# Kernel optimization log

Measured on AMD Instinct MI355X. Metric: run time of the kernel, lower is better.

The kernel has to match this reference:

```python
import jax, jax.numpy as jnp
import numpy as np

B, S, DM, NH, DK, DFF = 4, 2048, 512, 8, 64, 2048
EPS = 1e-5


def setup_inputs() -> dict:
    key = jax.random.key(0)
    ks = jax.random.split(key, 16)
    sd = 1.0 / np.sqrt(DM)
    inp = {
        'x': jax.random.normal(ks[0], (B, S, DM), dtype=jnp.float32),
        'wq': jax.random.normal(ks[1], (DM, DM), dtype=jnp.float32) * sd,
        'bq': jnp.zeros((DM,), dtype=jnp.float32),
        'wk': jax.random.normal(ks[2], (DM, DM), dtype=jnp.float32) * sd,
        'bk': jnp.zeros((DM,), dtype=jnp.float32),
        'wv': jax.random.normal(ks[3], (DM, DM), dtype=jnp.float32) * sd,
        'bv': jnp.zeros((DM,), dtype=jnp.float32),
        'wo': jax.random.normal(ks[4], (DM, DM), dtype=jnp.float32) * sd,
        'bo': jnp.zeros((DM,), dtype=jnp.float32),
        'ln_g': jnp.ones((DM,), dtype=jnp.float32),
        'ln_b': jnp.zeros((DM,), dtype=jnp.float32),
        'w1': jax.random.normal(ks[5], (DFF, DM), dtype=jnp.float32) * sd,
        'b1': jnp.zeros((DFF,), dtype=jnp.float32),
        'w2': jax.random.normal(ks[6], (DM, DFF), dtype=jnp.float32) * (1.0 / np.sqrt(DFF)),
        'b2': jnp.zeros((DM,), dtype=jnp.float32),
    }
    return inp


def _layernorm(x, g, b):
    mu = jnp.mean(x, axis=-1, keepdims=True)
    var = jnp.mean(jnp.square(x - mu), axis=-1, keepdims=True)
    return (x - mu) * jax.lax.rsqrt(var + EPS) * g + b


def reference(x, wq, bq, wk, bk, wv, bv, wo, bo, ln_g, ln_b, w1, b1, w2, b2):
    # projections (torch Linear: y = x @ W.T + b)
    q = x @ wq.T + bq
    k = x @ wk.T + bk
    v = x @ wv.T + bv
    # chunk along feature dim into NH heads of size DK
    q = q.reshape(B, S, NH, DK)
    k = k.reshape(B, S, NH, DK)
    v = v.reshape(B, S, NH, DK)
    scores = jnp.einsum('bihd,bjhd->bhij', q, k) / np.sqrt(DK)  # [B,NH,S,S]
    probs = jax.nn.softmax(scores, axis=-1)
    o = jnp.einsum('bhij,bjhd->bihd', probs, v).reshape(B, S, DM)
    o = o @ wo.T + bo
    # residual + shared layernorm (dropout p=0 -> identity)
    h = _layernorm(o + x, ln_g, ln_b)
    ff = jax.nn.relu(h @ w1.T + b1) @ w2.T + b2
    return _layernorm(ff + h, ln_g, ln_b)
```

## Files before the change

kernel.cpp:

```cpp
#include <hip/hip_runtime.h>

typedef __attribute__((ext_vector_type(8))) short short8;
typedef __attribute__((ext_vector_type(8))) unsigned short ushort8;
typedef __attribute__((ext_vector_type(4))) unsigned short ushort4v;
typedef __attribute__((ext_vector_type(4))) float f32x4;
typedef __attribute__((ext_vector_type(16))) float f32x16;

#define DEV static __device__ __forceinline__

DEV unsigned short f2bf(float f) {
  unsigned u = __builtin_bit_cast(unsigned, f);
  u += 0x7fffu + ((u >> 16) & 1u);
  return (unsigned short)(u >> 16);
}

DEV float bf2f(unsigned short u) {
  return __builtin_bit_cast(float, (unsigned)u << 16);
}

DEV void gload_lds16(const void* g, void* l) {
  __builtin_amdgcn_global_load_lds((__attribute__((address_space(1))) void*)g,
                                   (__attribute__((address_space(3))) void*)l,
                                   16, 0, 0);
}

DEV unsigned cvtpk(float lo, float hi) {
  unsigned u;
  asm("v_cvt_pk_bf16_f32 %0, %1, %2" : "=v"(u) : "v"(lo), "v"(hi));
  return u;
}

DEV void pl32(unsigned& a, unsigned& b) {
  asm("v_permlane32_swap_b32 %0, %1" : "+v"(a), "+v"(b));
}

DEV short8 pack4(unsigned a, unsigned b, unsigned c, unsigned d) {
  int4 t = make_int4((int)a, (int)b, (int)c, (int)d);
  return __builtin_bit_cast(short8, t);
}

__global__ __launch_bounds__(256) void cvt_all_k(
    const float4* __restrict__ wq, const float4* __restrict__ wk,
    const float4* __restrict__ wv, const float4* __restrict__ wo,
    const float4* __restrict__ w1, const float4* __restrict__ w2,
    const float4* __restrict__ x, ushort4v* __restrict__ wqkv,
    ushort4v* __restrict__ wob, ushort4v* __restrict__ w1b,
    ushort4v* __restrict__ w2b, ushort4v* __restrict__ xb) {
  const int i = threadIdx.x;
  const int b = blockIdx.x;
  const float4* s;
  ushort4v* d;
  size_t u;
  if (b < 256)       { s = wq; d = wqkv;          u = (size_t)b * 256 + i; }
  else if (b < 512)  { s = wk; d = wqkv + 65536;  u = (size_t)(b - 256) * 256 + i; }
  else if (b < 768)  { s = wv; d = wqkv + 131072; u = (size_t)(b - 512) * 256 + i; }
  else if (b < 1024) { s = wo; d = wob;           u = (size_t)(b - 768) * 256 + i; }
  else if (b < 2048) { s = w1; d = w1b;           u = (size_t)(b - 1024) * 256 + i; }
  else if (b < 3072) { s = w2; d = w2b;           u = (size_t)(b - 2048) * 256 + i; }
  else               { s = x;  d = xb;            u = (size_t)(b - 3072) * 256 + i; }
  float4 v = s[u];
  ushort4v o = { f2bf(v.x), f2bf(v.y), f2bf(v.z), f2bf(v.w) };
  d[u] = o;
}

__global__ void pack_bias_k(const float* __restrict__ bq, const float* __restrict__ bk,
                            const float* __restrict__ bv, float* __restrict__ o) {
  int i = threadIdx.x;
  o[i] = bq[i];
  o[512 + i] = bk[i];
  o[1024 + i] = bv[i];
}

template <int EPI>
__global__ __launch_bounds__(256) void gemm_bt(
    const unsigned short* __restrict__ A, const unsigned short* __restrict__ Bw,
    const float* __restrict__ bias, int M, int N, int K,
    unsigned short* __restrict__ outb, float* __restrict__ outf,
    const unsigned short* __restrict__ residb) {
  __shared__ __align__(16) unsigned short As[128 * 64];
  __shared__ __align__(16) unsigned short Bs[128 * 64];
  const int tid = threadIdx.x;
  const int lane = tid & 63;
  const int wv = tid >> 6;
  const int wr = wv >> 1, wc = wv & 1;
  const int lrow = lane & 15, lgrp = lane >> 4;
  const int bm = blockIdx.x * 128;
  const int bn = blockIdx.y * 128;

  f32x4 acc[4][4];
#pragma unroll
  for (int m = 0; m < 4; m++)
#pragma unroll
    for (int n = 0; n < 4; n++) acc[m][n] = (f32x4){0.f, 0.f, 0.f, 0.f};

  for (int k0 = 0; k0 < K; k0 += 64) {
    __syncthreads();
#pragma unroll
    for (int i = 0; i < 4; i++) {
      const int sb = wv * 64 + i * 256;
      const int slot = sb + lane;
      const int row = slot >> 3;
      const int cc = (slot & 7) ^ (row & 7);
      gload_lds16(A + (size_t)(bm + row) * K + k0 + cc * 8, &As[sb * 8]);
      gload_lds16(Bw + (size_t)(bn + row) * K + k0 + cc * 8, &Bs[sb * 8]);
    }
    __syncthreads();

#pragma unroll
    for (int kk = 0; kk < 2; kk++) {
      short8 af[4], bfr[4];
#pragma unroll
      for (int m = 0; m < 4; m++) {
        const int row = wr * 64 + m * 16 + lrow;
        af[m] = *(const short8*)&As[row * 64 + (((lgrp + 4 * kk) ^ (row & 7)) * 8)];
      }
#pragma unroll
      for (int n = 0; n < 4; n++) {
        const int row = wc * 64 + n * 16 + lrow;
        bfr[n] = *(const short8*)&Bs[row * 64 + (((lgrp + 4 * kk) ^ (row & 7)) * 8)];
      }
#pragma unroll
      for (int m = 0; m < 4; m++)
#pragma unroll
        for (int n = 0; n < 4; n++)
          acc[m][n] = __builtin_amdgcn_mfma_f32_16x16x32_bf16(af[m], bfr[n], acc[m][n], 0, 0, 0);
    }
  }

  if constexpr (EPI == 0) {
    const int proj = bn >> 9;
    if (proj == 2) {
      __shared__ __align__(16) unsigned short VT[128 * 136];
#pragma unroll
      for (int n = 0; n < 4; n++) {
        const int cl = wc * 64 + n * 16 + lrow;
        const float bval = bias[bn + cl];
#pragma unroll
        for (int m = 0; m < 4; m++)
#pragma unroll
          for (int r = 0; r < 4; r++)
            VT[cl * 136 + wr * 64 + m * 16 + lgrp * 4 + r] = f2bf(acc[m][n][r] + bval);
      }
      __syncthreads();
      const int j = (bn - 1024) >> 7;
      const int b = bm >> 11;
      const int sbase = bm & 2047;
      unsigned short* vout = outb + (size_t)2 * 4194304;
#pragma unroll
      for (int q = 0; q < 8; q++) {
        const int chunk = q * 256 + tid;
        const int cl = chunk >> 4, s8 = chunk & 15;
        const int head = 2 * j + (cl >> 6), d = cl & 63;
        ushort8 val = *(const ushort8*)&VT[cl * 136 + s8 * 8];
        *(ushort8*)(vout + ((size_t)(b * 8 + head) * 64 + d) * 2048 + sbase + s8 * 8) = val;
      }
    } else {
      const float qs = (proj == 0) ? 0.18033688011f : 1.0f;
#pragma unroll
      for (int m = 0; m < 4; m++) {
#pragma unroll
        for (int n = 0; n < 4; n++) {
          const int gcol = bn + wc * 64 + n * 16 + lrow;
          const float bval = bias[gcol];
          const int feat = gcol & 511;
          const int head = feat >> 6, d = feat & 63;
#pragma unroll
          for (int r = 0; r < 4; r++) {
            const int grow = bm + wr * 64 + m * 16 + lgrp * 4 + r;
            const int b = grow >> 11, s = grow & 2047;
            const int bh = b * 8 + head;
            outb[(size_t)proj * 4194304 + ((size_t)bh * 2048 + s) * 64 + d] =
                f2bf((acc[m][n][r] + bval) * qs);
          }
        }
      }
    }
  } else {
#pragma unroll
    for (int m = 0; m < 4; m++) {
#pragma unroll
      for (int n = 0; n < 4; n++) {
        const int gcol = bn + wc * 64 + n * 16 + lrow;
        const float bval = bias[gcol];
#pragma unroll
        for (int r = 0; r < 4; r++) {
          const int grow = bm + wr * 64 + m * 16 + lgrp * 4 + r;
          float v = acc[m][n][r] + bval;
          const size_t o = (size_t)grow * N + gcol;
          if constexpr (EPI == 1) {
            outb[o] = f2bf(v + bf2f(residb[o]));
          } else if constexpr (EPI == 2) {
            outb[o] = f2bf(v > 0.f ? v : 0.f);
          } else {
            outf[o] = v + bf2f(residb[o]);
          }
        }
      }
    }
  }
}

template <int EPI>
__global__ __launch_bounds__(256) void gemm_n64(
    const unsigned short* __restrict__ A, const unsigned short* __restrict__ Bw,
    const float* __restrict__ bias, int M, int N, int K,
    unsigned short* __restrict__ outb, float* __restrict__ outf,
    const unsigned short* __restrict__ residb) {
  __shared__ __align__(16) unsigned short As[128 * 64];
  __shared__ __align__(16) unsigned short Bs[64 * 64];
  const int tid = threadIdx.x;
  const int lane = tid & 63;
  const int wv = tid >> 6;
  const int lrow = lane & 15, lgrp = lane >> 4;
  const int bm = blockIdx.x * 128;
  const int bn = blockIdx.y * 64;

  f32x4 acc[2][4];
#pragma unroll
  for (int m = 0; m < 2; m++)
#pragma unroll
    for (int n = 0; n < 4; n++) acc[m][n] = (f32x4){0.f, 0.f, 0.f, 0.f};

  for (int k0 = 0; k0 < K; k0 += 64) {
    __syncthreads();
#pragma unroll
    for (int i = 0; i < 4; i++) {
      const int sb = wv * 64 + i * 256;
      const int slot = sb + lane;
      const int row = slot >> 3;
      const int cc = (slot & 7) ^ (row & 7);
      gload_lds16(A + (size_t)(bm + row) * K + k0 + cc * 8, &As[sb * 8]);
    }
#pragma unroll
    for (int i = 0; i < 2; i++) {
      const int sb = wv * 64 + i * 256;
      const int slot = sb + lane;
      const int row = slot >> 3;
      const int cc = (slot & 7) ^ (row & 7);
      gload_lds16(Bw + (size_t)(bn + row) * K + k0 + cc * 8, &Bs[sb * 8]);
    }
    __syncthreads();

#pragma unroll
    for (int kk = 0; kk < 2; kk++) {
      short8 af[2], bfr[4];
#pragma unroll
      for (int m = 0; m < 2; m++) {
        const int row = wv * 32 + m * 16 + lrow;
        af[m] = *(const short8*)&As[row * 64 + (((lgrp + 4 * kk) ^ (row & 7)) * 8)];
      }
#pragma unroll
      for (int n = 0; n < 4; n++) {
        const int row = n * 16 + lrow;
        bfr[n] = *(const short8*)&Bs[row * 64 + (((lgrp + 4 * kk) ^ (row & 7)) * 8)];
      }
#pragma unroll
      for (int m = 0; m < 2; m++)
#pragma unroll
        for (int n = 0; n < 4; n++)
          acc[m][n] = __builtin_amdgcn_mfma_f32_16x16x32_bf16(af[m], bfr[n], acc[m][n], 0, 0, 0);
    }
  }

#pragma unroll
  for (int m = 0; m < 2; m++) {
#pragma unroll
    for (int n = 0; n < 4; n++) {
      const int gcol = bn + n * 16 + lrow;
      const float bval = bias[gcol];
#pragma unroll
      for (int r = 0; r < 4; r++) {
        const int grow = bm + wv * 32 + m * 16 + lgrp * 4 + r;
        float v = acc[m][n][r] + bval;
        const size_t o = (size_t)grow * N + gcol;
        if constexpr (EPI == 1) {
          outb[o] = f2bf(v + bf2f(residb[o]));
        } else {
          outf[o] = v + bf2f(residb[o]);
        }
      }
    }
  }
}

__global__ __launch_bounds__(256) void attn_k(
    const unsigned short* __restrict__ Qg, const unsigned short* __restrict__ Kg,
    const unsigned short* __restrict__ Vg, unsigned short* __restrict__ Og) {
  __shared__ __align__(16) unsigned short Kl[2][64 * 64];
  __shared__ __align__(16) unsigned short Vl[2][64 * 64];
  const int tid = threadIdx.x, lane = tid & 63, wq = tid >> 6;
  const int ql = lane & 31;
  const int hi = lane >> 5;
  const int bid = blockIdx.x;
  const int lin = (bid & 7) * 64 + (bid >> 3);
  const int bh = lin >> 4;
  const int q0 = (lin & 15) * 128;
  const int qw = q0 + wq * 32;
  const size_t hbase = (size_t)bh * (2048 * 64);

  const int sb0 = wq * 64, sb1 = wq * 64 + 256;
  const int r0s = (sb0 + lane) >> 3, c0s = ((sb0 + lane) & 7) ^ (r0s & 7);
  const int r1s = (sb1 + lane) >> 3, c1s = ((sb1 + lane) & 7) ^ (r1s & 7);

  short8 qreg[4];
  {
    const unsigned short* qp = Qg + hbase + (size_t)(qw + ql) * 64 + hi * 8;
#pragma unroll
    for (int i = 0; i < 4; i++) qreg[i] = *(const short8*)(qp + 16 * i);
  }

  f32x16 oac0 = {0.f, 0.f, 0.f, 0.f, 0.f, 0.f, 0.f, 0.f,
                 0.f, 0.f, 0.f, 0.f, 0.f, 0.f, 0.f, 0.f};
  f32x16 oac1 = oac0;
  float lr = 0.f;

  gload_lds16(Kg + hbase + (size_t)r0s * 64 + c0s * 8, &Kl[0][sb0 * 8]);
  gload_lds16(Vg + hbase + (size_t)r0s * 2048 + c0s * 8, &Vl[0][sb0 * 8]);
  gload_lds16(Kg + hbase + (size_t)r1s * 64 + c1s * 8, &Kl[0][sb1 * 8]);
  gload_lds16(Vg + hbase + (size_t)r1s * 2048 + c1s * 8, &Vl[0][sb1 * 8]);
  __syncthreads();

  for (int it = 0; it < 32; ++it) {
    const int cur = it & 1;
    if (it < 31) {
      const int kt = (it + 1) * 64;
      const int nxt = cur ^ 1;
      gload_lds16(Kg + hbase + (size_t)(kt + r0s) * 64 + c0s * 8, &Kl[nxt][sb0 * 8]);
      gload_lds16(Vg + hbase + (size_t)r0s * 2048 + kt + c0s * 8, &Vl[nxt][sb0 * 8]);
      gload_lds16(Kg + hbase + (size_t)(kt + r1s) * 64 + c1s * 8, &Kl[nxt][sb1 * 8]);
      gload_lds16(Vg + hbase + (size_t)r1s * 2048 + kt + c1s * 8, &Vl[nxt][sb1 * 8]);
    }

    f32x16 sc0 = {0.f, 0.f, 0.f, 0.f, 0.f, 0.f, 0.f, 0.f,
                  0.f, 0.f, 0.f, 0.f, 0.f, 0.f, 0.f, 0.f};
    f32x16 sc1 = sc0;
    __builtin_amdgcn_s_setprio(1);
#pragma unroll
    for (int i = 0; i < 4; i++) {
      const int c8 = 2 * i + hi;
      const int r0 = ql;
      const int r1 = ql + 32;
      short8 ka = *(const short8*)&Kl[cur][(r0 * 8 + (c8 ^ (r0 & 7))) * 8];
      short8 kb = *(const short8*)&Kl[cur][(r1 * 8 + (c8 ^ (r1 & 7))) * 8];
      sc0 = __builtin_amdgcn_mfma_f32_32x32x16_bf16(ka, qreg[i], sc0, 0, 0, 0);
      sc1 = __builtin_amdgcn_mfma_f32_32x32x16_bf16(kb, qreg[i], sc1, 0, 0, 0);
    }
    __builtin_amdgcn_s_setprio(0);

    short8 pa[4];
#pragma unroll
    for (int t2 = 0; t2 < 2; t2++) {
      const f32x16& sc = t2 ? sc1 : sc0;
      float p[16];
#pragma unroll
      for (int r = 0; r < 16; r++) {
        p[r] = __builtin_amdgcn_exp2f(sc[r]);
        lr += p[r];
      }
      unsigned w0a = cvtpk(p[0], p[1]),   w0b = cvtpk(p[2], p[3]);
      unsigned w1a = cvtpk(p[4], p[5]),   w1b = cvtpk(p[6], p[7]);
      unsigned w2a = cvtpk(p[8], p[9]),   w2b = cvtpk(p[10], p[11]);
      unsigned w3a = cvtpk(p[12], p[13]), w3b = cvtpk(p[14], p[15]);
      pl32(w0a, w1a);
      pl32(w0b, w1b);
      pa[2 * t2] = pack4(w0a, w0b, w1a, w1b);
      pl32(w2a, w3a);
      pl32(w2b, w3b);
      pa[2 * t2 + 1] = pack4(w2a, w2b, w3a, w3b);
    }

    __builtin_amdgcn_s_setprio(1);
#pragma unroll
    for (int ks = 0; ks < 4; ks++) {
      const int c8 = 2 * ks + hi;
      const int r0 = ql;
      const int r1 = ql + 32;
      short8 vb0 = *(const short8*)&Vl[cur][(r0 * 8 + (c8 ^ (r0 & 7))) * 8];
      short8 vb1 = *(const short8*)&Vl[cur][(r1 * 8 + (c8 ^ (r1 & 7))) * 8];
      oac0 = __builtin_amdgcn_mfma_f32_32x32x16_bf16(pa[ks], vb0, oac0, 0, 0, 0);
      oac1 = __builtin_amdgcn_mfma_f32_32x32x16_bf16(pa[ks], vb1, oac1, 0, 0, 0);
    }
    __builtin_amdgcn_s_setprio(0);

    __syncthreads();
  }

  lr += __shfl_xor(lr, 32);
  const float inv = 1.0f / lr;

  const int b = bh >> 3, h = bh & 7;
#pragma unroll
  for (int r = 0; r < 16; r++) {
    const int qrow = (r & 3) + 8 * (r >> 2) + 4 * hi;
    const float invr = __shfl(inv, qrow);
    const size_t base = ((size_t)(b * 2048 + qw + qrow)) * 512 + h * 64 + ql;
    Og[base] = f2bf(oac0[r] * invr);
    Og[base + 32] = f2bf(oac1[r] * invr);
  }
}

__global__ __launch_bounds__(64) void ln_k(const float* __restrict__ in,
                                           const float* __restrict__ g,
                                           const float* __restrict__ bb,
                                           float* __restrict__ outf) {
  const int row = blockIdx.x, lane = threadIdx.x;
  const float4* p = (const float4*)(in + (size_t)row * 512);
  float4 a = p[lane], b4 = p[lane + 64];
  float s = a.x + a.y + a.z + a.w + b4.x + b4.y + b4.z + b4.w;
#pragma unroll
  for (int off = 32; off >= 1; off >>= 1) s += __shfl_xor(s, off);
  const float mu = s * (1.f / 512.f);
  float q = 0.f;
  {
    float d;
    d = a.x - mu; q += d * d; d = a.y - mu; q += d * d;
    d = a.z - mu; q += d * d; d = a.w - mu; q += d * d;
    d = b4.x - mu; q += d * d; d = b4.y - mu; q += d * d;
    d = b4.z - mu; q += d * d; d = b4.w - mu; q += d * d;
  }
#pragma unroll
  for (int off = 32; off >= 1; off >>= 1) q += __shfl_xor(q, off);
  const float rstd = rsqrtf(q * (1.f / 512.f) + 1e-5f);
  const float4* gp = (const float4*)g;
  const float4* bp = (const float4*)bb;
  float4 g0 = gp[lane], g1 = gp[lane + 64], c0 = bp[lane], c1 = bp[lane + 64];
  float4 o0, o1;
  o0.x = (a.x - mu) * rstd * g0.x + c0.x;
  o0.y = (a.y - mu) * rstd * g0.y + c0.y;
  o0.z = (a.z - mu) * rstd * g0.z + c0.z;
  o0.w = (a.w - mu) * rstd * g0.w + c0.w;
  o1.x = (b4.x - mu) * rstd * g1.x + c1.x;
  o1.y = (b4.y - mu) * rstd * g1.y + c1.y;
  o1.z = (b4.z - mu) * rstd * g1.z + c1.z;
  o1.w = (b4.w - mu) * rstd * g1.w + c1.w;
  float4* of = (float4*)(outf + (size_t)row * 512);
  of[lane] = o0;
  of[lane + 64] = o1;
}

__global__ __launch_bounds__(64) void ln_bf_k(const unsigned short* __restrict__ in,
                                              const float* __restrict__ g,
                                              const float* __restrict__ bb,
                                              unsigned short* __restrict__ out) {
  const int row = blockIdx.x, lane = threadIdx.x;
  ushort8 v = *(const ushort8*)(in + (size_t)row * 512 + lane * 8);
  float f[8];
#pragma unroll
  for (int j = 0; j < 8; j++) f[j] = bf2f(v[j]);
  float s = 0.f;
#pragma unroll
  for (int j = 0; j < 8; j++) s += f[j];
#pragma unroll
  for (int off = 32; off >= 1; off >>= 1) s += __shfl_xor(s, off);
  const float mu = s * (1.f / 512.f);
  float q = 0.f;
#pragma unroll
  for (int j = 0; j < 8; j++) { const float d = f[j] - mu; q += d * d; }
#pragma unroll
  for (int off = 32; off >= 1; off >>= 1) q += __shfl_xor(q, off);
  const float rstd = rsqrtf(q * (1.f / 512.f) + 1e-5f);
  const float4* gp = (const float4*)g;
  const float4* bp = (const float4*)bb;
  float4 g0 = gp[lane * 2], g1 = gp[lane * 2 + 1];
  float4 c0 = bp[lane * 2], c1 = bp[lane * 2 + 1];
  const float gg[8] = {g0.x, g0.y, g0.z, g0.w, g1.x, g1.y, g1.z, g1.w};
  const float cc[8] = {c0.x, c0.y, c0.z, c0.w, c1.x, c1.y, c1.z, c1.w};
  ushort8 ov;
#pragma unroll
  for (int j = 0; j < 8; j++) ov[j] = f2bf((f[j] - mu) * rstd * gg[j] + cc[j]);
  *(ushort8*)(out + (size_t)row * 512 + lane * 8) = ov;
}

extern "C" void kernel_launch(void* const* d_in, const int* in_sizes, int n_in,
                              void* d_out, int out_size, void* d_ws, size_t ws_size,
                              hipStream_t stream) {
  const float* x = (const float*)d_in[0];
  const float* wq = (const float*)d_in[1];
  const float* bq = (const float*)d_in[2];
  const float* wk = (const float*)d_in[3];
  const float* bk = (const float*)d_in[4];
  const float* wv = (const float*)d_in[5];
  const float* bv = (const float*)d_in[6];
  const float* wo = (const float*)d_in[7];
  const float* bo = (const float*)d_in[8];
  const float* ln_g = (const float*)d_in[9];
  const float* ln_b = (const float*)d_in[10];
  const float* w1 = (const float*)d_in[11];
  const float* b1 = (const float*)d_in[12];
  const float* w2 = (const float*)d_in[13];
  const float* b2 = (const float*)d_in[14];

  unsigned short* ws_u = (unsigned short*)d_ws;
  unsigned short* wqkv = ws_u;
  unsigned short* wob = wqkv + 786432;
  unsigned short* w1b = wob + 262144;
  unsigned short* w2b = w1b + 1048576;
  unsigned short* xb = w2b + 1048576;
  unsigned short* qb = xb + 4194304;
  unsigned short* kb = qb + 4194304;
  unsigned short* vtb = kb + 4194304;
  unsigned short* ob = vtb + 4194304;
  unsigned short* s1b = ob + 4194304;
  unsigned short* hb = s1b + 4194304;
  unsigned short* f1b = qb;
  float* bqkv = (float*)(hb + 4194304);

  cvt_all_k<<<7168, 256, 0, stream>>>(
      (const float4*)wq, (const float4*)wk, (const float4*)wv, (const float4*)wo,
      (const float4*)w1, (const float4*)w2, (const float4*)x,
      (ushort4v*)wqkv, (ushort4v*)wob, (ushort4v*)w1b, (ushort4v*)w2b,
      (ushort4v*)xb);
  pack_bias_k<<<1, 512, 0, stream>>>(bq, bk, bv, bqkv);

  gemm_bt<0><<<dim3(64, 12), 256, 0, stream>>>(xb, wqkv, bqkv, 8192, 1536, 512,
                                               qb, nullptr, nullptr);
  attn_k<<<512, 256, 0, stream>>>(qb, kb, vtb, ob);
  gemm_n64<1><<<dim3(64, 8), 256, 0, stream>>>(ob, wob, bo, 8192, 512, 512,
                                               s1b, nullptr, xb);
  ln_bf_k<<<8192, 64, 0, stream>>>(s1b, ln_g, ln_b, hb);
  gemm_bt<2><<<dim3(64, 16), 256, 0, stream>>>(hb, w1b, b1, 8192, 2048, 512,
                                               f1b, nullptr, nullptr);
  gemm_n64<3><<<dim3(64, 8), 256, 0, stream>>>(f1b, w2b, b2, 8192, 512, 2048,
                                               nullptr, (float*)d_out, hb);
  ln_k<<<8192, 64, 0, stream>>>((float*)d_out, ln_g, ln_b, (float*)d_out);
}
```

Before: 170.7 us.

## Split attention KV range across two blocks and add a combine kernel

The attention kernel now splits each query tile's 2048-key range into two halves handled by separate blocks, doubling the grid from 512 to 1024 blocks. Each block writes unnormalized partial outputs (bf16) and partial row sums to a workspace. A new combine kernel adds the two partials, divides by the summed denominators, and writes the final head-interleaved output. This aims to improve CU occupancy and load balance, at the cost of an extra launch, extra global traffic for the partials, and an extra bf16 rounding of the unnormalized partials.

```diff
diff --git a/kernel.cpp b/kernel.cpp
--- a/kernel.cpp
+++ b/kernel.cpp
@@ -285,16 +285,20 @@
 
 __global__ __launch_bounds__(256) void attn_k(
     const unsigned short* __restrict__ Qg, const unsigned short* __restrict__ Kg,
-    const unsigned short* __restrict__ Vg, unsigned short* __restrict__ Og) {
+    const unsigned short* __restrict__ Vg, unsigned short* __restrict__ pO,
+    float* __restrict__ pL) {
   __shared__ __align__(16) unsigned short Kl[2][64 * 64];
   __shared__ __align__(16) unsigned short Vl[2][64 * 64];
   const int tid = threadIdx.x, lane = tid & 63, wq = tid >> 6;
   const int ql = lane & 31;
   const int hi = lane >> 5;
   const int bid = blockIdx.x;
-  const int lin = (bid & 7) * 64 + (bid >> 3);
-  const int bh = lin >> 4;
-  const int q0 = (lin & 15) * 128;
+  const int lin = (bid & 7) * 128 + (bid >> 3);
+  const int bh = lin >> 5;
+  const int rest = lin & 31;
+  const int q0 = (rest >> 1) * 128;
+  const int sp = rest & 1;
+  const int kbase = sp * 1024;
   const int qw = q0 + wq * 32;
   const size_t hbase = (size_t)bh * (2048 * 64);
 
@@ -314,16 +318,16 @@
   f32x16 oac1 = oac0;
   float lr = 0.f;
 
-  gload_lds16(Kg + hbase + (size_t)r0s * 64 + c0s * 8, &Kl[0][sb0 * 8]);
-  gload_lds16(Vg + hbase + (size_t)r0s * 2048 + c0s * 8, &Vl[0][sb0 * 8]);
-  gload_lds16(Kg + hbase + (size_t)r1s * 64 + c1s * 8, &Kl[0][sb1 * 8]);
-  gload_lds16(Vg + hbase + (size_t)r1s * 2048 + c1s * 8, &Vl[0][sb1 * 8]);
+  gload_lds16(Kg + hbase + (size_t)(kbase + r0s) * 64 + c0s * 8, &Kl[0][sb0 * 8]);
+  gload_lds16(Vg + hbase + (size_t)r0s * 2048 + kbase + c0s * 8, &Vl[0][sb0 * 8]);
+  gload_lds16(Kg + hbase + (size_t)(kbase + r1s) * 64 + c1s * 8, &Kl[0][sb1 * 8]);
+  gload_lds16(Vg + hbase + (size_t)r1s * 2048 + kbase + c1s * 8, &Vl[0][sb1 * 8]);
   __syncthreads();
 
-  for (int it = 0; it < 32; ++it) {
+  for (int it = 0; it < 16; ++it) {
     const int cur = it & 1;
-    if (it < 31) {
-      const int kt = (it + 1) * 64;
+    if (it < 15) {
+      const int kt = kbase + (it + 1) * 64;
       const int nxt = cur ^ 1;
       gload_lds16(Kg + hbase + (size_t)(kt + r0s) * 64 + c0s * 8, &Kl[nxt][sb0 * 8]);
       gload_lds16(Vg + hbase + (size_t)r0s * 2048 + kt + c0s * 8, &Vl[nxt][sb0 * 8]);
@@ -386,17 +390,34 @@
   }
 
   lr += __shfl_xor(lr, 32);
-  const float inv = 1.0f / lr;
-
-  const int b = bh >> 3, h = bh & 7;
+  if (hi == 0) pL[((size_t)bh * 2048 + qw + ql) * 2 + sp] = lr;
+
 #pragma unroll
   for (int r = 0; r < 16; r++) {
     const int qrow = (r & 3) + 8 * (r >> 2) + 4 * hi;
-    const float invr = __shfl(inv, qrow);
-    const size_t base = ((size_t)(b * 2048 + qw + qrow)) * 512 + h * 64 + ql;
-    Og[base] = f2bf(oac0[r] * invr);
-    Og[base + 32] = f2bf(oac1[r] * invr);
-  }
+    const size_t base = (((size_t)bh * 2048 + qw + qrow) * 2 + sp) * 64 + ql;
+    pO[base] = f2bf(oac0[r]);
+    pO[base + 32] = f2bf(oac1[r]);
+  }
+}
+
+__global__ __launch_bounds__(256) void attn_combine_k(
+    const unsigned short* __restrict__ pO, const float* __restrict__ pL,
+    unsigned short* __restrict__ ob) {
+  const int c = blockIdx.x * 256 + threadIdx.x;
+  const int row = c >> 6, col8 = c & 63;
+  const int h = col8 >> 3, d8 = col8 & 7;
+  const int b = row >> 11, s = row & 2047;
+  const int bh = b * 8 + h;
+  const size_t qb = (size_t)bh * 2048 + s;
+  const size_t base = qb * 128 + d8 * 8;
+  ushort8 a = *(const ushort8*)(pO + base);
+  ushort8 bb8 = *(const ushort8*)(pO + base + 64);
+  const float inv = 1.0f / (pL[qb * 2] + pL[qb * 2 + 1]);
+  ushort8 o;
+#pragma unroll
+  for (int j = 0; j < 8; j++) o[j] = f2bf((bf2f(a[j]) + bf2f(bb8[j])) * inv);
+  *(ushort8*)(ob + (size_t)row * 512 + col8 * 8) = o;
 }
 
 __global__ __launch_bounds__(64) void ln_k(const float* __restrict__ in,
@@ -504,6 +525,8 @@
   unsigned short* hb = s1b + 4194304;
   unsigned short* f1b = qb;
   float* bqkv = (float*)(hb + 4194304);
+  unsigned short* pO = (unsigned short*)(bqkv + 1536);
+  float* pL = (float*)(pO + 8388608);
 
   cvt_all_k<<<7168, 256, 0, stream>>>(
       (const float4*)wq, (const float4*)wk, (const float4*)wv, (const float4*)wo,
@@ -514,7 +537,8 @@
 
   gemm_bt<0><<<dim3(64, 12), 256, 0, stream>>>(xb, wqkv, bqkv, 8192, 1536, 512,
                                                qb, nullptr, nullptr);
-  attn_k<<<512, 256, 0, stream>>>(qb, kb, vtb, ob);
+  attn_k<<<1024, 256, 0, stream>>>(qb, kb, vtb, pO, pL);
+  attn_combine_k<<<2048, 256, 0, stream>>>(pO, pL, ob);
   gemm_n64<1><<<dim3(64, 8), 256, 0, stream>>>(ob, wob, bo, 8192, 512, 512,
                                                s1b, nullptr, xb);
   ln_bf_k<<<8192, 64, 0, stream>>>(s1b, ln_g, ln_b, hb);
```

New measurement: 176.2 us. 1.03x slower.
